# Kernel optimization log

Hardware: AMD Instinct MI355X
Metric: run time of the kernel (lower is better)

The kernel has to match this reference:

```python
import jax, jax.numpy as jnp
import numpy as np

B, T, C = 2, 2048, 2048
N_HEAD = 16
HS = C // N_HEAD
D_LATENT = C // 2


def setup_inputs() -> dict:
    key = jax.random.key(0)
    ks = jax.random.split(key, 7)
    s = 0.02
    return {
        "x": jax.random.normal(ks[0], (B, T, C), dtype=jnp.float32),
        "Wq": jax.random.normal(ks[1], (C, C), dtype=jnp.float32) * s,
        "Wc": jax.random.normal(ks[2], (C, D_LATENT), dtype=jnp.float32) * s,
        "Wk": jax.random.normal(ks[3], (D_LATENT, C), dtype=jnp.float32) * s,
        "Wv": jax.random.normal(ks[4], (D_LATENT, C), dtype=jnp.float32) * s,
        "Wo": jax.random.normal(ks[5], (C, C), dtype=jnp.float32) * s,
        "bo": jnp.zeros((C,), dtype=jnp.float32),
    }


def reference(x, Wq, Wc, Wk, Wv, Wo, bo):
    b, t, c = x.shape
    # projections (torch Linear without bias, weights stored as (in, out))
    q = x @ Wq                    # (B,T,C)
    c_latent = x @ Wc             # (B,T,d_latent)
    k = c_latent @ Wk             # (B,T,C)
    v = c_latent @ Wv             # (B,T,C)
    # split heads -> (B,H,T,hs)
    q = q.reshape(b, t, N_HEAD, HS).transpose(0, 2, 1, 3)
    k = k.reshape(b, t, N_HEAD, HS).transpose(0, 2, 1, 3)
    v = v.reshape(b, t, N_HEAD, HS).transpose(0, 2, 1, 3)
    scale = 1.0 / jnp.sqrt(jnp.asarray(HS, dtype=x.dtype))
    scores = jnp.einsum('bhqd,bhkd->bhqk', q, k) * scale
    causal = jnp.tril(jnp.ones((t, t), dtype=bool))
    scores = jnp.where(causal, scores, jnp.finfo(scores.dtype).min)
    attn = jax.nn.softmax(scores, axis=-1)
    y = jnp.einsum('bhqk,bhkd->bhqd', attn, v)      # (B,H,T,hs)
    y = y.transpose(0, 2, 1, 3).reshape(b, t, c)
    return y @ Wo + bo
```

## Files before the change

kernel.cpp:

```cpp
#include <hip/hip_runtime.h>
#include <hip/hip_bf16.h>
#include <math.h>

typedef __hip_bfloat16 bf16;
typedef __attribute__((ext_vector_type(8))) short bf16x8;
typedef __attribute__((ext_vector_type(4))) float f32x4;

#define B_  2
#define T_  2048
#define C_  2048
#define H_  16
#define HS_ 128
#define DL_ 1024
#define M_  (B_ * T_)
#define NQT_ (T_ / 128)

__device__ inline void lds16(const bf16* g, bf16* l) {
    __builtin_amdgcn_global_load_lds(
        (const __attribute__((address_space(1))) void*)g,
        (__attribute__((address_space(3))) void*)l, 16, 0, 0);
}

__global__ __launch_bounds__(256) void cast_bf16_k(
    const float* __restrict__ in, bf16* __restrict__ out)
{
    const size_t i = ((size_t)blockIdx.x * 256 + threadIdx.x) * 8;
    const float4 a = *(const float4*)(in + i);
    const float4 b = *(const float4*)(in + i + 4);
    bf16 o[8];
    o[0] = __float2bfloat16(a.x); o[1] = __float2bfloat16(a.y);
    o[2] = __float2bfloat16(a.z); o[3] = __float2bfloat16(a.w);
    o[4] = __float2bfloat16(b.x); o[5] = __float2bfloat16(b.y);
    o[6] = __float2bfloat16(b.z); o[7] = __float2bfloat16(b.w);
    *(uint4*)(out + i) = *(const uint4*)o;
}

__global__ __launch_bounds__(256) void transpose_cast(
    const float* __restrict__ in, bf16* __restrict__ out, int R, int Cc)
{
    __shared__ float t[32][33];
    const int bx = blockIdx.x * 32, by = blockIdx.y * 32;
    const int tx = threadIdx.x & 31, ty = threadIdx.x >> 5;
#pragma unroll
    for (int i = 0; i < 32; i += 8)
        t[ty + i][tx] = in[(size_t)(by + ty + i) * Cc + bx + tx];
    __syncthreads();
#pragma unroll
    for (int i = 0; i < 32; i += 8)
        out[(size_t)(bx + ty + i) * R + by + tx] = __float2bfloat16(t[tx][ty + i]);
}

__global__ __launch_bounds__(256) void gemm_bt_mfma(
    const bf16* __restrict__ A, const bf16* __restrict__ Bt,
    bf16* __restrict__ Cbf, float* __restrict__ Cf32,
    const float* __restrict__ bias, int M, int N, int K)
{
    __shared__ __align__(16) bf16 As[128 * 32];
    __shared__ __align__(16) bf16 Bs[128 * 32];
    const int tid  = threadIdx.x;
    const int lane = tid & 63;
    const int wave = tid >> 6;
    const int wm = wave >> 1, wn = wave & 1;
    const int quad = lane >> 4, l16 = lane & 15;
    const int sw = (l16 >> 1) & 3;
    const int m0 = blockIdx.y * 128, n0 = blockIdx.x * 128;

    f32x4 acc[4][4];
#pragma unroll
    for (int i = 0; i < 4; i++)
#pragma unroll
        for (int j = 0; j < 4; j++) acc[i][j] = (f32x4){0.f, 0.f, 0.f, 0.f};

    const int r0  = tid >> 2;
    const int kcs = (((tid & 3) ^ ((r0 >> 1) & 3)) * 8);
    const bf16* Ap = A  + (size_t)(m0 + r0) * K + kcs;
    const bf16* Bp = Bt + (size_t)(n0 + r0) * K + kcs;
    const size_t rstr = (size_t)64 * K;

    for (int k0 = 0; k0 < K; k0 += 32) {
        if (k0) __syncthreads();
        lds16(Ap + k0,        As + tid * 8);
        lds16(Ap + rstr + k0, As + 2048 + tid * 8);
        lds16(Bp + k0,        Bs + tid * 8);
        lds16(Bp + rstr + k0, Bs + 2048 + tid * 8);
        __syncthreads();

        bf16x8 af[4], bfr[4];
#pragma unroll
        for (int mi = 0; mi < 4; mi++)
            af[mi] = *(const bf16x8*)&As[(wm * 64 + mi * 16 + l16) * 32 + (quad ^ sw) * 8];
#pragma unroll
        for (int ni = 0; ni < 4; ni++)
            bfr[ni] = *(const bf16x8*)&Bs[(wn * 64 + ni * 16 + l16) * 32 + (quad ^ sw) * 8];
#pragma unroll
        for (int mi = 0; mi < 4; mi++)
#pragma unroll
            for (int ni = 0; ni < 4; ni++)
                acc[mi][ni] = __builtin_amdgcn_mfma_f32_16x16x32_bf16(
                    af[mi], bfr[ni], acc[mi][ni], 0, 0, 0);
    }

#pragma unroll
    for (int mi = 0; mi < 4; mi++) {
#pragma unroll
        for (int ni = 0; ni < 4; ni++) {
            const int col = n0 + wn * 64 + ni * 16 + l16;
#pragma unroll
            for (int r = 0; r < 4; r++) {
                const int row = m0 + wm * 64 + mi * 16 + quad * 4 + r;
                if (Cf32)
                    Cf32[(size_t)row * N + col] = acc[mi][ni][r] + bias[col];
                else
                    Cbf[(size_t)row * N + col] = __float2bfloat16(acc[mi][ni][r]);
            }
        }
    }
}

__global__ __launch_bounds__(256) void gemm_qc_fused(
    const bf16* __restrict__ A, const bf16* __restrict__ Bt,
    bf16* __restrict__ Cq, bf16* __restrict__ Cc, int M, int K)
{
    __shared__ __align__(16) bf16 As[128 * 32];
    __shared__ __align__(16) bf16 Bs[128 * 32];
    const int tid  = threadIdx.x;
    const int lane = tid & 63;
    const int wave = tid >> 6;
    const int wm = wave >> 1, wn = wave & 1;
    const int quad = lane >> 4, l16 = lane & 15;
    const int sw = (l16 >> 1) & 3;
    const int m0 = blockIdx.y * 128, n0 = blockIdx.x * 128;

    f32x4 acc[4][4];
#pragma unroll
    for (int i = 0; i < 4; i++)
#pragma unroll
        for (int j = 0; j < 4; j++) acc[i][j] = (f32x4){0.f, 0.f, 0.f, 0.f};

    const int r0  = tid >> 2;
    const int kcs = (((tid & 3) ^ ((r0 >> 1) & 3)) * 8);
    const bf16* Ap = A  + (size_t)(m0 + r0) * K + kcs;
    const bf16* Bp = Bt + (size_t)(n0 + r0) * K + kcs;
    const size_t rstr = (size_t)64 * K;

    for (int k0 = 0; k0 < K; k0 += 32) {
        if (k0) __syncthreads();
        lds16(Ap + k0,        As + tid * 8);
        lds16(Ap + rstr + k0, As + 2048 + tid * 8);
        lds16(Bp + k0,        Bs + tid * 8);
        lds16(Bp + rstr + k0, Bs + 2048 + tid * 8);
        __syncthreads();

        bf16x8 af[4], bfr[4];
#pragma unroll
        for (int mi = 0; mi < 4; mi++)
            af[mi] = *(const bf16x8*)&As[(wm * 64 + mi * 16 + l16) * 32 + (quad ^ sw) * 8];
#pragma unroll
        for (int ni = 0; ni < 4; ni++)
            bfr[ni] = *(const bf16x8*)&Bs[(wn * 64 + ni * 16 + l16) * 32 + (quad ^ sw) * 8];
#pragma unroll
        for (int mi = 0; mi < 4; mi++)
#pragma unroll
            for (int ni = 0; ni < 4; ni++)
                acc[mi][ni] = __builtin_amdgcn_mfma_f32_16x16x32_bf16(
                    af[mi], bfr[ni], acc[mi][ni], 0, 0, 0);
    }

    const bool is_q = (n0 < C_);
    const float scl = is_q ? 0.08838834764831845f : 1.0f;
    bf16* dst = is_q ? Cq : Cc;
    const int ld   = is_q ? C_ : DL_;
    const int coff = is_q ? 0 : C_;
#pragma unroll
    for (int mi = 0; mi < 4; mi++) {
#pragma unroll
        for (int ni = 0; ni < 4; ni++) {
            const int col = n0 - coff + wn * 64 + ni * 16 + l16;
#pragma unroll
            for (int r = 0; r < 4; r++) {
                const int row = m0 + wm * 64 + mi * 16 + quad * 4 + r;
                dst[(size_t)row * ld + col] = __float2bfloat16(acc[mi][ni][r] * scl);
            }
        }
    }
}

__global__ __launch_bounds__(512) void flash_paired(
    const bf16* __restrict__ Q, const bf16* __restrict__ K,
    const bf16* __restrict__ Vt, bf16* __restrict__ Y)
{
    __shared__ __align__(16) bf16 Ks[4][64][32];
    __shared__ __align__(16) bf16 Vs[2][128][32];
    __shared__ __align__(16) bf16 Ps[8][32][72];
    const int tid  = threadIdx.x;
    const int lane = tid & 63, wv = tid >> 6;
    const int g = wv >> 2, w4 = wv & 3;
    const int quad = lane >> 4, l16 = lane & 15;
    const int sw = (l16 >> 1) & 3;
    const int pa = blockIdx.x;
    const int h = blockIdx.y, b = blockIdx.z;
    const int qt = g ? (NQT_ - 1 - pa) : pa;
    const int q0 = qt * 128;
    const int jmax_own = 2 * qt + 2;
    const int jmax = 2 * (NQT_ - 1 - pa) + 2;

    const int t2  = tid & 255;
    const int hi  = tid >> 8;
    const int sr  = t2 >> 2;
    const int ssl = ((t2 & 3) ^ ((sr >> 1) & 3)) * 8;

    bf16x8 qf[2][4];
#pragma unroll
    for (int mi = 0; mi < 2; mi++) {
        const size_t rowQ = (size_t)(b * T_ + q0 + w4 * 32 + mi * 16 + l16) * C_ + h * HS_;
#pragma unroll
        for (int c = 0; c < 4; c++)
            qf[mi][c] = *(const bf16x8*)(Q + rowQ + c * 32 + quad * 8);
    }

    f32x4 oacc[2][8];
#pragma unroll
    for (int mi = 0; mi < 2; mi++)
#pragma unroll
        for (int dt = 0; dt < 8; dt++) oacc[mi][dt] = (f32x4){0.f, 0.f, 0.f, 0.f};
    float l_s[2][4] = {{0.f,0.f,0.f,0.f},{0.f,0.f,0.f,0.f}};

    for (int j = 0; j < jmax; j++) {
        const int kv0 = j * 64;
        if (j) __syncthreads();
#pragma unroll
        for (int kc = 0; kc < 2; kc++)
            lds16(K + (size_t)(b * T_ + kv0 + sr) * C_ + h * HS_ + (hi + 2 * kc) * 32 + ssl,
                  &Ks[hi + 2 * kc][0][0] + t2 * 8);
#pragma unroll
        for (int hf = 0; hf < 2; hf++)
            lds16(Vt + (size_t)(h * HS_ + hf * 64 + sr) * M_ + b * T_ + kv0 + hi * 32 + ssl,
                  &Vs[hi][hf * 64][0] + t2 * 8);
        __syncthreads();

        if (j < jmax_own) {
            const bool act0 = (kv0 <= q0 + w4 * 32 + 15);
            const bool act1 = (kv0 <= q0 + w4 * 32 + 31);
            f32x4 sacc[2][4];
#pragma unroll
            for (int mi = 0; mi < 2; mi++)
#pragma unroll
                for (int nt = 0; nt < 4; nt++) sacc[mi][nt] = (f32x4){0.f, 0.f, 0.f, 0.f};
#pragma unroll
            for (int c = 0; c < 4; c++) {
                bf16x8 kf[4];
#pragma unroll
                for (int nt = 0; nt < 4; nt++)
                    kf[nt] = *(const bf16x8*)&Ks[c][nt * 16 + l16][(quad ^ sw) * 8];
                if (act0)
#pragma unroll
                    for (int nt = 0; nt < 4; nt++)
                        sacc[0][nt] = __builtin_amdgcn_mfma_f32_16x16x32_bf16(
                            qf[0][c], kf[nt], sacc[0][nt], 0, 0, 0);
                if (act1)
#pragma unroll
                    for (int nt = 0; nt < 4; nt++)
                        sacc[1][nt] = __builtin_amdgcn_mfma_f32_16x16x32_bf16(
                            qf[1][c], kf[nt], sacc[1][nt], 0, 0, 0);
            }
#pragma unroll
            for (int mi = 0; mi < 2; mi++) {
                const bool act = mi ? act1 : act0;
                if (!act) continue;
                const int rowbase = q0 + w4 * 32 + mi * 16;
                float p[4][4];
                if (kv0 + 63 > rowbase) {
#pragma unroll
                    for (int nt = 0; nt < 4; nt++)
#pragma unroll
                        for (int r = 0; r < 4; r++) {
                            const int col = kv0 + nt * 16 + l16;
                            const int row = rowbase + quad * 4 + r;
                            p[nt][r] = (col <= row) ? __expf(sacc[mi][nt][r]) : 0.f;
                        }
                } else {
#pragma unroll
                    for (int nt = 0; nt < 4; nt++)
#pragma unroll
                        for (int r = 0; r < 4; r++)
                            p[nt][r] = __expf(sacc[mi][nt][r]);
                }
#pragma unroll
                for (int r = 0; r < 4; r++)
                    l_s[mi][r] += p[0][r] + p[1][r] + p[2][r] + p[3][r];
#pragma unroll
                for (int nt = 0; nt < 4; nt++)
#pragma unroll
                    for (int r = 0; r < 4; r++)
                        Ps[wv][mi * 16 + quad * 4 + r][nt * 16 + l16] = __float2bfloat16(p[nt][r]);
            }
            bf16x8 pab[2][2];
#pragma unroll
            for (int mi = 0; mi < 2; mi++) {
                pab[mi][0] = *(const bf16x8*)&Ps[wv][mi * 16 + l16][quad * 8];
                pab[mi][1] = *(const bf16x8*)&Ps[wv][mi * 16 + l16][32 + quad * 8];
            }
#pragma unroll
            for (int dt = 0; dt < 8; dt++) {
                const bf16x8 vf0 = *(const bf16x8*)&Vs[0][dt * 16 + l16][(quad ^ sw) * 8];
                const bf16x8 vf1 = *(const bf16x8*)&Vs[1][dt * 16 + l16][(quad ^ sw) * 8];
                if (act0) {
                    oacc[0][dt] = __builtin_amdgcn_mfma_f32_16x16x32_bf16(pab[0][0], vf0, oacc[0][dt], 0, 0, 0);
                    oacc[0][dt] = __builtin_amdgcn_mfma_f32_16x16x32_bf16(pab[0][1], vf1, oacc[0][dt], 0, 0, 0);
                }
                if (act1) {
                    oacc[1][dt] = __builtin_amdgcn_mfma_f32_16x16x32_bf16(pab[1][0], vf0, oacc[1][dt], 0, 0, 0);
                    oacc[1][dt] = __builtin_amdgcn_mfma_f32_16x16x32_bf16(pab[1][1], vf1, oacc[1][dt], 0, 0, 0);
                }
            }
        }
    }

#pragma unroll
    for (int mi = 0; mi < 2; mi++) {
        float inv[4];
#pragma unroll
        for (int r = 0; r < 4; r++) {
            float l = l_s[mi][r];
            l += __shfl_xor(l, 1);
            l += __shfl_xor(l, 2);
            l += __shfl_xor(l, 4);
            l += __shfl_xor(l, 8);
            inv[r] = 1.f / l;
        }
        const int rowbase = q0 + w4 * 32 + mi * 16;
#pragma unroll
        for (int dt = 0; dt < 8; dt++)
#pragma unroll
            for (int r = 0; r < 4; r++)
                Y[(size_t)(b * T_ + rowbase + quad * 4 + r) * C_ + h * HS_ + dt * 16 + l16] =
                    __float2bfloat16(oacc[mi][dt][r] * inv[r]);
    }
}

extern "C" void kernel_launch(void* const* d_in, const int* in_sizes, int n_in,
                              void* d_out, int out_size, void* d_ws, size_t ws_size,
                              hipStream_t stream) {
    const float* x  = (const float*)d_in[0];
    const float* Wq = (const float*)d_in[1];
    const float* Wc = (const float*)d_in[2];
    const float* Wk = (const float*)d_in[3];
    const float* Wv = (const float*)d_in[4];
    const float* Wo = (const float*)d_in[5];
    const float* bo = (const float*)d_in[6];
    float* out = (float*)d_out;

    bf16* ws   = (bf16*)d_ws;
    bf16* x_bf = ws;
    bf16* Wq_t = x_bf + (size_t)M_ * C_;
    bf16* Wc_t = Wq_t + (size_t)C_ * C_;
    bf16* Wk_t = Wc_t + (size_t)DL_ * C_;
    bf16* Wv_t = Wk_t + (size_t)C_ * DL_;
    bf16* Wo_t = Wv_t + (size_t)C_ * DL_;
    bf16* q    = Wo_t + (size_t)C_ * C_;
    bf16* clat = q    + (size_t)M_ * C_;
    bf16* kk   = clat + (size_t)M_ * DL_;
    bf16* vt   = kk   + (size_t)M_ * C_;
    bf16* y    = vt   + (size_t)C_ * M_;

    const dim3 blk(256);

    cast_bf16_k<<<dim3((M_ * C_) / (256 * 8)), blk, 0, stream>>>(x, x_bf);
    transpose_cast<<<dim3(C_ / 32,  C_ / 32),  blk, 0, stream>>>(Wq, Wq_t, C_,  C_);
    transpose_cast<<<dim3(DL_ / 32, C_ / 32),  blk, 0, stream>>>(Wc, Wc_t, C_,  DL_);
    transpose_cast<<<dim3(C_ / 32,  DL_ / 32), blk, 0, stream>>>(Wk, Wk_t, DL_, C_);
    transpose_cast<<<dim3(C_ / 32,  DL_ / 32), blk, 0, stream>>>(Wv, Wv_t, DL_, C_);
    transpose_cast<<<dim3(C_ / 32,  C_ / 32),  blk, 0, stream>>>(Wo, Wo_t, C_,  C_);

    gemm_qc_fused<<<dim3((C_ + DL_) / 128, M_ / 128), blk, 0, stream>>>(
        x_bf, Wq_t, q, clat, M_, C_);
    gemm_bt_mfma<<<dim3(C_ / 128, M_ / 128), blk, 0, stream>>>(
        clat, Wk_t, kk, nullptr, nullptr, M_, C_, DL_);
    gemm_bt_mfma<<<dim3(M_ / 128, C_ / 128), blk, 0, stream>>>(
        Wv_t, clat, vt, nullptr, nullptr, C_, M_, DL_);

    flash_paired<<<dim3(NQT_ / 2, H_, B_), dim3(512), 0, stream>>>(q, kk, vt, y);

    gemm_bt_mfma<<<dim3(C_ / 128, M_ / 128), blk, 0, stream>>>(
        y, Wo_t, nullptr, out, bo, M_, C_, C_);
}
```

Baseline: 395.9 us.

## Double GEMM K-tile to 64, merge weight transposes, remap flash block order

The GEMM kernels now stage a 64-wide K slice per iteration with an 8-way XOR swizzle, which halves the number of barrier pairs and doubles the MFMA work per sync. It also doubles LDS use per block, which may reduce occupancy. The five weight transpose-cast launches are merged into one launch indexed by blockIdx.z, with early exit for the out-of-range tiles of the smaller matrices. The flash attention grid is flattened, and block IDs are remapped so that consecutive blocks span different batch and head pairs, changing scheduling and L2 locality.

```diff
diff --git a/kernel.cpp b/kernel.cpp
--- a/kernel.cpp
+++ b/kernel.cpp
@@ -35,11 +35,24 @@
     *(uint4*)(out + i) = *(const uint4*)o;
 }
 
-__global__ __launch_bounds__(256) void transpose_cast(
-    const float* __restrict__ in, bf16* __restrict__ out, int R, int Cc)
+__global__ __launch_bounds__(256) void transpose_cast5(
+    const float* __restrict__ s0, const float* __restrict__ s1,
+    const float* __restrict__ s2, const float* __restrict__ s3,
+    const float* __restrict__ s4,
+    bf16* __restrict__ d0, bf16* __restrict__ d1, bf16* __restrict__ d2,
+    bf16* __restrict__ d3, bf16* __restrict__ d4)
 {
+    const float* in; bf16* out; int R, Cc;
+    switch (blockIdx.z) {
+        case 0: in = s0; out = d0; R = C_;  Cc = C_;  break;
+        case 1: in = s1; out = d1; R = C_;  Cc = DL_; break;
+        case 2: in = s2; out = d2; R = DL_; Cc = C_;  break;
+        case 3: in = s3; out = d3; R = DL_; Cc = C_;  break;
+        default: in = s4; out = d4; R = C_; Cc = C_;  break;
+    }
+    const int bx = blockIdx.x * 32, by = blockIdx.y * 32;
+    if (bx >= Cc || by >= R) return;
     __shared__ float t[32][33];
-    const int bx = blockIdx.x * 32, by = blockIdx.y * 32;
     const int tx = threadIdx.x & 31, ty = threadIdx.x >> 5;
 #pragma unroll
     for (int i = 0; i < 32; i += 8)
@@ -55,14 +68,14 @@
     bf16* __restrict__ Cbf, float* __restrict__ Cf32,
     const float* __restrict__ bias, int M, int N, int K)
 {
-    __shared__ __align__(16) bf16 As[128 * 32];
-    __shared__ __align__(16) bf16 Bs[128 * 32];
+    __shared__ __align__(16) bf16 As[128 * 64];
+    __shared__ __align__(16) bf16 Bs[128 * 64];
     const int tid  = threadIdx.x;
     const int lane = tid & 63;
     const int wave = tid >> 6;
     const int wm = wave >> 1, wn = wave & 1;
     const int quad = lane >> 4, l16 = lane & 15;
-    const int sw = (l16 >> 1) & 3;
+    const int sw8 = (l16 >> 1) & 7;
     const int m0 = blockIdx.y * 128, n0 = blockIdx.x * 128;
 
     f32x4 acc[4][4];
@@ -71,33 +84,39 @@
 #pragma unroll
         for (int j = 0; j < 4; j++) acc[i][j] = (f32x4){0.f, 0.f, 0.f, 0.f};
 
-    const int r0  = tid >> 2;
-    const int kcs = (((tid & 3) ^ ((r0 >> 1) & 3)) * 8);
-    const bf16* Ap = A  + (size_t)(m0 + r0) * K + kcs;
-    const bf16* Bp = Bt + (size_t)(n0 + r0) * K + kcs;
-    const size_t rstr = (size_t)64 * K;
-
-    for (int k0 = 0; k0 < K; k0 += 32) {
+    const int srow = tid >> 3;
+    const int ssl  = (((tid & 7) ^ ((srow >> 1) & 7)) * 8);
+    const bf16* Ap = A  + (size_t)(m0 + srow) * K + ssl;
+    const bf16* Bp = Bt + (size_t)(n0 + srow) * K + ssl;
+    const size_t rstr = (size_t)32 * K;
+
+    for (int k0 = 0; k0 < K; k0 += 64) {
         if (k0) __syncthreads();
-        lds16(Ap + k0,        As + tid * 8);
-        lds16(Ap + rstr + k0, As + 2048 + tid * 8);
-        lds16(Bp + k0,        Bs + tid * 8);
-        lds16(Bp + rstr + k0, Bs + 2048 + tid * 8);
+#pragma unroll
+        for (int ii = 0; ii < 4; ii++) {
+            lds16(Ap + ii * rstr + k0, As + ii * 2048 + tid * 8);
+            lds16(Bp + ii * rstr + k0, Bs + ii * 2048 + tid * 8);
+        }
         __syncthreads();
 
-        bf16x8 af[4], bfr[4];
-#pragma unroll
-        for (int mi = 0; mi < 4; mi++)
-            af[mi] = *(const bf16x8*)&As[(wm * 64 + mi * 16 + l16) * 32 + (quad ^ sw) * 8];
-#pragma unroll
-        for (int ni = 0; ni < 4; ni++)
-            bfr[ni] = *(const bf16x8*)&Bs[(wn * 64 + ni * 16 + l16) * 32 + (quad ^ sw) * 8];
-#pragma unroll
-        for (int mi = 0; mi < 4; mi++)
+#pragma unroll
+        for (int w = 0; w < 2; w++) {
+            bf16x8 af[4], bfr[4];
+#pragma unroll
+            for (int mi = 0; mi < 4; mi++)
+                af[mi] = *(const bf16x8*)&As[(wm * 64 + mi * 16 + l16) * 64 +
+                                            (((w << 2) | quad) ^ sw8) * 8];
 #pragma unroll
             for (int ni = 0; ni < 4; ni++)
-                acc[mi][ni] = __builtin_amdgcn_mfma_f32_16x16x32_bf16(
-                    af[mi], bfr[ni], acc[mi][ni], 0, 0, 0);
+                bfr[ni] = *(const bf16x8*)&Bs[(wn * 64 + ni * 16 + l16) * 64 +
+                                              (((w << 2) | quad) ^ sw8) * 8];
+#pragma unroll
+            for (int mi = 0; mi < 4; mi++)
+#pragma unroll
+                for (int ni = 0; ni < 4; ni++)
+                    acc[mi][ni] = __builtin_amdgcn_mfma_f32_16x16x32_bf16(
+                        af[mi], bfr[ni], acc[mi][ni], 0, 0, 0);
+        }
     }
 
 #pragma unroll
@@ -121,14 +140,14 @@
     const bf16* __restrict__ A, const bf16* __restrict__ Bt,
     bf16* __restrict__ Cq, bf16* __restrict__ Cc, int M, int K)
 {
-    __shared__ __align__(16) bf16 As[128 * 32];
-    __shared__ __align__(16) bf16 Bs[128 * 32];
+    __shared__ __align__(16) bf16 As[128 * 64];
+    __shared__ __align__(16) bf16 Bs[128 * 64];
     const int tid  = threadIdx.x;
     const int lane = tid & 63;
     const int wave = tid >> 6;
     const int wm = wave >> 1, wn = wave & 1;
     const int quad = lane >> 4, l16 = lane & 15;
-    const int sw = (l16 >> 1) & 3;
+    const int sw8 = (l16 >> 1) & 7;
     const int m0 = blockIdx.y * 128, n0 = blockIdx.x * 128;
 
     f32x4 acc[4][4];
@@ -137,33 +156,39 @@
 #pragma unroll
         for (int j = 0; j < 4; j++) acc[i][j] = (f32x4){0.f, 0.f, 0.f, 0.f};
 
-    const int r0  = tid >> 2;
-    const int kcs = (((tid & 3) ^ ((r0 >> 1) & 3)) * 8);
-    const bf16* Ap = A  + (size_t)(m0 + r0) * K + kcs;
-    const bf16* Bp = Bt + (size_t)(n0 + r0) * K + kcs;
-    const size_t rstr = (size_t)64 * K;
-
-    for (int k0 = 0; k0 < K; k0 += 32) {
+    const int srow = tid >> 3;
+    const int ssl  = (((tid & 7) ^ ((srow >> 1) & 7)) * 8);
+    const bf16* Ap = A  + (size_t)(m0 + srow) * K + ssl;
+    const bf16* Bp = Bt + (size_t)(n0 + srow) * K + ssl;
+    const size_t rstr = (size_t)32 * K;
+
+    for (int k0 = 0; k0 < K; k0 += 64) {
         if (k0) __syncthreads();
-        lds16(Ap + k0,        As + tid * 8);
-        lds16(Ap + rstr + k0, As + 2048 + tid * 8);
-        lds16(Bp + k0,        Bs + tid * 8);
-        lds16(Bp + rstr + k0, Bs + 2048 + tid * 8);
+#pragma unroll
+        for (int ii = 0; ii < 4; ii++) {
+            lds16(Ap + ii * rstr + k0, As + ii * 2048 + tid * 8);
+            lds16(Bp + ii * rstr + k0, Bs + ii * 2048 + tid * 8);
+        }
         __syncthreads();
 
-        bf16x8 af[4], bfr[4];
-#pragma unroll
-        for (int mi = 0; mi < 4; mi++)
-            af[mi] = *(const bf16x8*)&As[(wm * 64 + mi * 16 + l16) * 32 + (quad ^ sw) * 8];
-#pragma unroll
-        for (int ni = 0; ni < 4; ni++)
-            bfr[ni] = *(const bf16x8*)&Bs[(wn * 64 + ni * 16 + l16) * 32 + (quad ^ sw) * 8];
-#pragma unroll
-        for (int mi = 0; mi < 4; mi++)
+#pragma unroll
+        for (int w = 0; w < 2; w++) {
+            bf16x8 af[4], bfr[4];
+#pragma unroll
+            for (int mi = 0; mi < 4; mi++)
+                af[mi] = *(const bf16x8*)&As[(wm * 64 + mi * 16 + l16) * 64 +
+                                            (((w << 2) | quad) ^ sw8) * 8];
 #pragma unroll
             for (int ni = 0; ni < 4; ni++)
-                acc[mi][ni] = __builtin_amdgcn_mfma_f32_16x16x32_bf16(
-                    af[mi], bfr[ni], acc[mi][ni], 0, 0, 0);
+                bfr[ni] = *(const bf16x8*)&Bs[(wn * 64 + ni * 16 + l16) * 64 +
+                                              (((w << 2) | quad) ^ sw8) * 8];
+#pragma unroll
+            for (int mi = 0; mi < 4; mi++)
+#pragma unroll
+                for (int ni = 0; ni < 4; ni++)
+                    acc[mi][ni] = __builtin_amdgcn_mfma_f32_16x16x32_bf16(
+                        af[mi], bfr[ni], acc[mi][ni], 0, 0, 0);
+        }
     }
 
     const bool is_q = (n0 < C_);
@@ -197,8 +222,10 @@
     const int g = wv >> 2, w4 = wv & 3;
     const int quad = lane >> 4, l16 = lane & 15;
     const int sw = (l16 >> 1) & 3;
-    const int pa = blockIdx.x;
-    const int h = blockIdx.y, b = blockIdx.z;
+    const int bid = blockIdx.x;
+    const int bh = (bid & 7) * 4 + ((bid >> 3) & 3);
+    const int pa = bid >> 5;
+    const int b = bh >> 4, h = bh & 15;
     const int qt = g ? (NQT_ - 1 - pa) : pa;
     const int q0 = qt * 128;
     const int jmax_own = 2 * qt + 2;
@@ -366,11 +393,8 @@
     const dim3 blk(256);
 
     cast_bf16_k<<<dim3((M_ * C_) / (256 * 8)), blk, 0, stream>>>(x, x_bf);
-    transpose_cast<<<dim3(C_ / 32,  C_ / 32),  blk, 0, stream>>>(Wq, Wq_t, C_,  C_);
-    transpose_cast<<<dim3(DL_ / 32, C_ / 32),  blk, 0, stream>>>(Wc, Wc_t, C_,  DL_);
-    transpose_cast<<<dim3(C_ / 32,  DL_ / 32), blk, 0, stream>>>(Wk, Wk_t, DL_, C_);
-    transpose_cast<<<dim3(C_ / 32,  DL_ / 32), blk, 0, stream>>>(Wv, Wv_t, DL_, C_);
-    transpose_cast<<<dim3(C_ / 32,  C_ / 32),  blk, 0, stream>>>(Wo, Wo_t, C_,  C_);
+    transpose_cast5<<<dim3(C_ / 32, C_ / 32, 5), blk, 0, stream>>>(
+        Wq, Wc, Wk, Wv, Wo, Wq_t, Wc_t, Wk_t, Wv_t, Wo_t);
 
     gemm_qc_fused<<<dim3((C_ + DL_) / 128, M_ / 128), blk, 0, stream>>>(
         x_bf, Wq_t, q, clat, M_, C_);
@@ -379,7 +403,7 @@
     gemm_bt_mfma<<<dim3(M_ / 128, C_ / 128), blk, 0, stream>>>(
         Wv_t, clat, vt, nullptr, nullptr, C_, M_, DL_);
 
-    flash_paired<<<dim3(NQT_ / 2, H_, B_), dim3(512), 0, stream>>>(q, kk, vt, y);
+    flash_paired<<<dim3((NQT_ / 2) * H_ * B_), dim3(512), 0, stream>>>(q, kk, vt, y);
 
     gemm_bt_mfma<<<dim3(C_ / 128, M_ / 128), blk, 0, stream>>>(
         y, Wo_t, nullptr, out, bo, M_, C_, C_);
```

After: 369.3 us. -6.7%, faster.
